# Kernel optimization log

Hardware: AMD Instinct MI355X
Metric: run time of the kernel (lower is better)

Reference implementation:

```python
import jax, jax.numpy as jnp
import numpy as np

B, LTEXT, LVIS, D, H = 16, 128, 4096, 1024, 16
HD = D // H


def setup_inputs() -> dict:
    key = jax.random.key(0)
    ks = jax.random.split(key, 8)
    s = 0.02
    return {
        'hidden_states': jax.random.normal(ks[0], (B, LVIS, D), jnp.float32),
        'text_states': jax.random.normal(ks[1], (LTEXT, B, D), jnp.float32),
        'Wq': jax.random.normal(ks[2], (D, D), jnp.float32) * s,
        'bq': jnp.zeros((D,), jnp.float32),
        'Wk': jax.random.normal(ks[3], (D, D), jnp.float32) * s,
        'bk': jnp.zeros((D,), jnp.float32),
        'Wv': jax.random.normal(ks[4], (D, D), jnp.float32) * s,
        'bv': jnp.zeros((D,), jnp.float32),
        'Wo': jax.random.normal(ks[5], (D, D), jnp.float32) * s,
        'bo': jnp.zeros((D,), jnp.float32),
    }


def reference(hidden_states, text_states, Wq, bq, Wk, bk, Wv, bv, Wo, bo):
    # text_states: (L_text, B, D) -- code unpacks text_len, bsz from dims 0,1
    # hidden_states: (B, L_vis, D) -- key/value source
    Ltext, bsz, d = text_states.shape
    Lvis = hidden_states.shape[1]
    scale = HD ** -0.5

    # projections (torch Linear x @ W.T + b, here W stored already transposed)
    q = (text_states @ Wq + bq) * scale
    # faithful to torch .view: flatten memory then reshape to (B, Ltext, H, hd)
    q = q.reshape(bsz, Ltext, H, HD).transpose(0, 2, 1, 3)        # (B,H,Lt,hd)
    k = (hidden_states @ Wk + bk).reshape(bsz, Lvis, H, HD).transpose(0, 2, 1, 3)
    v = (hidden_states @ Wv + bv).reshape(bsz, Lvis, H, HD).transpose(0, 2, 1, 3)

    attn = jax.nn.softmax(jnp.einsum('bhtd,bhsd->bhts', q, k), axis=-1)  # (B,H,Lt,Lv)
    text_guided_vision = jnp.einsum('bhts,bhsd->bhtd', attn, v)          # (B,H,Lt,hd)
    # second matmul with transposed attention weights: P^T @ (P V)
    out = jnp.einsum('bhts,bhtd->bhsd', attn, text_guided_vision)        # (B,H,Lv,hd)

    out = out.transpose(0, 2, 1, 3).reshape(bsz, Lvis, d)
    return out @ Wo + bo
```

## Files before the change

kernel.cpp:

```cpp
#include <hip/hip_runtime.h>
#include <stdint.h>

typedef short  s16x8 __attribute__((ext_vector_type(8)));
typedef float  f32x4 __attribute__((ext_vector_type(4)));
typedef unsigned short u16x4 __attribute__((ext_vector_type(4)));

__device__ __forceinline__ unsigned short f2bf(float f) {
  unsigned u = __builtin_bit_cast(unsigned, f);
  u = (u + 0x7fffu + ((u >> 16) & 1u)) >> 16;
  return (unsigned short)u;
}

__device__ __forceinline__ void glds16(const void* g, void* l) {
  __builtin_amdgcn_global_load_lds((const __attribute__((address_space(1))) void*)g,
                                   (__attribute__((address_space(3))) void*)l, 16, 0, 0);
}

__device__ __forceinline__ f32x4 mfma16(s16x8 a, s16x8 b, f32x4 c) {
  return __builtin_amdgcn_mfma_f32_16x16x32_bf16(a, b, c, 0, 0, 0);
}

#define VM4 asm volatile("s_waitcnt vmcnt(4)" ::: "memory")
#define VM0 asm volatile("s_waitcnt vmcnt(0)" ::: "memory")

__global__ __launch_bounds__(256) void kt_cvt(const float* __restrict__ X,
                                              unsigned short* __restrict__ Y) {
  const size_t N8 = (size_t)16 * 4096 * 1024 / 8;
  for (size_t i = (size_t)blockIdx.x * 256 + threadIdx.x; i < N8;
       i += (size_t)gridDim.x * 256) {
    const float* g = X + i * 8;
    f32x4 a = *(const f32x4*)g;
    f32x4 b = *(const f32x4*)(g + 4);
    s16x8 o;
    o[0]=f2bf(a[0]); o[1]=f2bf(a[1]); o[2]=f2bf(a[2]); o[3]=f2bf(a[3]);
    o[4]=f2bf(b[0]); o[5]=f2bf(b[1]); o[6]=f2bf(b[2]); o[7]=f2bf(b[3]);
    *(s16x8*)(Y + i * 8) = o;
  }
}

__global__ void kt_transpose(const float* __restrict__ W, unsigned short* __restrict__ WT) {
  __shared__ float tile[64][65];
  int n0 = blockIdx.x * 64, k0 = blockIdx.y * 64;
  int tx = threadIdx.x, ty = threadIdx.y;
  #pragma unroll
  for (int r = ty; r < 64; r += 4)
    tile[r][tx] = W[(size_t)(k0 + r) * 1024 + n0 + tx];
  __syncthreads();
  #pragma unroll
  for (int r = ty; r < 64; r += 4)
    WT[(size_t)(n0 + r) * 1024 + k0 + tx] = f2bf(tile[tx][r]);
}

__global__ __launch_bounds__(256, 2) void kt_gemm_q(
    const float* __restrict__ Ain, const unsigned short* __restrict__ BT,
    const float* __restrict__ bias, unsigned short* __restrict__ Cout) {
  __shared__ __align__(16) unsigned short As[128 * 32];
  __shared__ __align__(16) unsigned short Bs[128 * 32];
  const int tid = threadIdx.x, lane = tid & 63, wave = tid >> 6;
  const int l15 = lane & 15, quad = lane >> 4;
  const int wr = wave >> 1, wc = wave & 1;
  const int n0 = blockIdx.x * 128, m0 = blockIdx.y * 128;

  f32x4 acc[4][4] = {};
  for (int k0 = 0; k0 < 1024; k0 += 32) {
    __syncthreads();
    #pragma unroll
    for (int i = 0; i < 2; ++i) {
      int rowb = (wave * 2 + i) * 16 + (lane >> 2);
      glds16(BT + (size_t)(n0 + rowb) * 1024 + k0 + (lane & 3) * 8,
             &Bs[(wave * 2 + i) * 512]);
    }
    {
      const float* A = Ain;
      int row = tid >> 1, ks = (tid & 1) * 16;
      const float* g = &A[(size_t)(m0 + row) * 1024 + k0 + ks];
      f32x4 fa = *(const f32x4*)(g);
      f32x4 fb = *(const f32x4*)(g + 4);
      f32x4 fc = *(const f32x4*)(g + 8);
      f32x4 fd = *(const f32x4*)(g + 12);
      s16x8 lo, hi;
      lo[0]=f2bf(fa[0]); lo[1]=f2bf(fa[1]); lo[2]=f2bf(fa[2]); lo[3]=f2bf(fa[3]);
      lo[4]=f2bf(fb[0]); lo[5]=f2bf(fb[1]); lo[6]=f2bf(fb[2]); lo[7]=f2bf(fb[3]);
      hi[0]=f2bf(fc[0]); hi[1]=f2bf(fc[1]); hi[2]=f2bf(fc[2]); hi[3]=f2bf(fc[3]);
      hi[4]=f2bf(fd[0]); hi[5]=f2bf(fd[1]); hi[6]=f2bf(fd[2]); hi[7]=f2bf(fd[3]);
      *(s16x8*)&As[row * 32 + ks] = lo;
      *(s16x8*)&As[row * 32 + ks + 8] = hi;
    }
    __syncthreads();
    s16x8 a[4], b[4];
    #pragma unroll
    for (int i = 0; i < 4; ++i) a[i] = *(const s16x8*)&As[(wr * 64 + i * 16 + l15) * 32 + quad * 8];
    #pragma unroll
    for (int j = 0; j < 4; ++j) b[j] = *(const s16x8*)&Bs[(wc * 64 + j * 16 + l15) * 32 + quad * 8];
    #pragma unroll
    for (int i = 0; i < 4; ++i)
      #pragma unroll
      for (int j = 0; j < 4; ++j) acc[i][j] = mfma16(a[i], b[j], acc[i][j]);
  }
  #pragma unroll
  for (int j = 0; j < 4; ++j) {
    int col = n0 + wc * 64 + j * 16 + l15;
    float bv = bias[col];
    #pragma unroll
    for (int i = 0; i < 4; ++i)
      #pragma unroll
      for (int r = 0; r < 4; ++r) {
        int row = m0 + wr * 64 + i * 16 + quad * 4 + r;
        float v = (acc[i][j][r] + bv) * 0.125f;
        size_t idx = ((size_t)((row >> 7) * 16 + (col >> 6)) * 128 + (row & 127)) * 64 + (col & 63);
        Cout[idx] = f2bf(v);
      }
  }
}

template <int MODE>
__global__ __launch_bounds__(512, 2) void kt_gemm256(
    const unsigned short* __restrict__ A, const unsigned short* __restrict__ BT,
    const float* __restrict__ bias0, const float* __restrict__ bias1,
    void* __restrict__ out0, void* __restrict__ out1) {
  constexpr int NN = (MODE == 0) ? 8 : 4;
  constexpr int CHUNK = (MODE == 0) ? 256 : 128;
  __shared__ __align__(16) unsigned short lds[65536];
  const int tid = threadIdx.x, lane = tid & 63, wave = tid >> 6;
  const int l15 = lane & 15, quad = lane >> 4;
  const int wr = wave >> 2, wc = wave & 3;
  const int r0 = lane >> 3, sck = (lane & 7) ^ r0;
  const int bid = blockIdx.x;
  const int logical = (bid & 7) * CHUNK + (bid >> 3);
  const int nblk = logical & (NN - 1), mblk = logical / NN;
  const int n0 = nblk * 256, m0 = mblk * 256;
  const unsigned short* Asrc = A + (size_t)m0 * 1024;
  const unsigned short* Bsrc = BT + (size_t)n0 * 1024;

  f32x4 acc[8][4] = {};
  s16x8 bf_[4][2];

  auto stageA = [&](int t, int h, int buf) {
    #pragma unroll
    for (int is = 0; is < 2; ++is) {
      int c = wave * 2 + is;
      glds16(Asrc + (size_t)(h * 128 + c * 8 + r0) * 1024 + t * 64 + sck * 8,
             &lds[buf * 32768 + h * 8192 + c * 512]);
    }
  };
  auto stageB = [&](int t, int h, int buf) {
    #pragma unroll
    for (int is = 0; is < 2; ++is) {
      int c = wave * 2 + is;
      glds16(Bsrc + (size_t)(h * 128 + c * 8 + r0) * 1024 + t * 64 + sck * 8,
             &lds[buf * 32768 + 16384 + h * 8192 + c * 512]);
    }
  };

  stageA(0, 0, 0); stageA(0, 1, 0); stageB(0, 0, 0); stageB(0, 1, 0);
  stageB(1, 0, 1); stageB(1, 1, 1);
  VM4;
  __builtin_amdgcn_s_barrier();

  #pragma unroll 1
  for (int it = 0; it < 8; ++it) {
    const bool last = (it == 7);
    const int te = 2 * it;
    #pragma unroll
    for (int half = 0; half < 2; ++half) {
      const int buf = half;
      #pragma unroll
      for (int p = 0; p < 4; ++p) {
        if (p == 0) {
          #pragma unroll
          for (int j = 0; j < 4; ++j)
            #pragma unroll
            for (int kk = 0; kk < 2; ++kk) {
              int r = (wc & 1) * 64 + j * 16 + l15;
              bf_[j][kk] = *(const s16x8*)&lds[buf * 32768 + 16384 + (wc >> 1) * 8192
                                               + r * 64 + (((kk * 4 + quad) ^ (r & 7)) << 3)];
            }
        }
        s16x8 af[2][2];
        #pragma unroll
        for (int ii = 0; ii < 2; ++ii)
          #pragma unroll
          for (int kk = 0; kk < 2; ++kk) {
            int r = (p * 2 + ii) * 16 + l15;
            af[ii][kk] = *(const s16x8*)&lds[buf * 32768 + wr * 8192
                                             + r * 64 + (((kk * 4 + quad) ^ (r & 7)) << 3)];
          }
        if (half == 0) {
          if (p == 0) { stageA(te + 1, 0, 1); stageA(te + 1, 1, 1); }
          else if (p == 1) { if (!last) stageB(te + 2, 0, 0); }
          else if (p == 2) { if (!last) stageB(te + 2, 1, 0); }
        } else {
          if (p == 0) { if (!last) stageA(te + 2, 0, 0); }
          else if (p == 1) { if (!last) { stageA(te + 2, 1, 0); stageB(te + 3, 0, 1); } }
          else if (p == 2) { if (!last) stageB(te + 3, 1, 1); }
        }
        __builtin_amdgcn_s_barrier();
        __builtin_amdgcn_s_setprio(1);
        #pragma unroll
        for (int ii = 0; ii < 2; ++ii)
          #pragma unroll
          for (int j = 0; j < 4; ++j)
            #pragma unroll
            for (int kk = 0; kk < 2; ++kk)
              acc[p * 2 + ii][j] = mfma16(af[ii][kk], bf_[j][kk], acc[p * 2 + ii][j]);
        __builtin_amdgcn_s_setprio(0);
        if (p == 3) {
          if (half == 0) { if (last) { VM0; } else { VM4; } }
          else           { if (!last) { VM4; } }
        }
        __builtin_amdgcn_s_barrier();
      }
    }
  }

  const int bb = m0 >> 12;
  const bool isV = (MODE == 0) && (n0 >= 1024);
  const float* bias = isV ? bias1 : bias0;
  #pragma unroll
  for (int j = 0; j < 4; ++j) {
    const int colg = n0 + wc * 64 + j * 16 + l15;
    const int c1 = colg & 1023;
    const float bv = bias[c1];
    const int hcol = c1 >> 6, dcol = c1 & 63;
    #pragma unroll
    for (int i = 0; i < 8; ++i) {
      const int row0 = m0 + wr * 128 + i * 16 + quad * 4;
      const int s = row0 & 4095;
      if constexpr (MODE == 0) {
        if (isV) {
          size_t base = (((size_t)bb * 16 + hcol) * 64 + dcol) * 4096 + s;
          u16x4 w;
          #pragma unroll
          for (int r = 0; r < 4; ++r) w[r] = f2bf(acc[i][j][r] + bv);
          *(u16x4*)&((unsigned short*)out1)[base] = w;
        } else {
          unsigned short* Ko = (unsigned short*)out0;
          size_t base = (((size_t)bb * 16 + hcol) * 4096 + s) * 64 + dcol;
          #pragma unroll
          for (int r = 0; r < 4; ++r) Ko[base + (size_t)r * 64] = f2bf(acc[i][j][r] + bv);
        }
      } else {
        float* O = (float*)out0;
        size_t base = (size_t)row0 * 1024 + colg;
        #pragma unroll
        for (int r = 0; r < 4; ++r) O[base + (size_t)r * 1024] = acc[i][j][r] + bv;
      }
    }
  }
}

__global__ __launch_bounds__(256, 2) void kt_attn1(
    const unsigned short* __restrict__ Qb, const unsigned short* __restrict__ Kb,
    const unsigned short* __restrict__ Vt, float* __restrict__ RpT,
    float* __restrict__ Zp) {
  __shared__ __align__(16) unsigned short Ks[128 * 64];
  __shared__ __align__(16) unsigned short Vts[64 * 128];
  __shared__ __align__(16) unsigned short Es[128 * 128];
  const int tid = threadIdx.x, lane = tid & 63, wave = tid >> 6;
  const int l15 = lane & 15, quad = lane >> 4;
  const int bid = blockIdx.x;
  const int lid = (bid & 7) * 128 + (bid >> 3);
  const int qidx = lid & 3, bh = lid >> 2;
  const size_t kbase = (size_t)bh * 4096 * 64;
  const size_t vbase = (size_t)bh * 64 * 4096;
  s16x8 qa[2][2];
  #pragma unroll
  for (int i = 0; i < 2; ++i)
    #pragma unroll
    for (int kk = 0; kk < 2; ++kk)
      qa[i][kk] = *(const s16x8*)&Qb[((size_t)bh * 128 + wave * 32 + i * 16 + l15) * 64 + kk * 32 + quad * 8];
  s16x8 bones;
  { unsigned short o = (l15 == 0) ? (unsigned short)0x3F80 : (unsigned short)0;
    #pragma unroll
    for (int c2 = 0; c2 < 8; ++c2) bones[c2] = (short)o; }
  f32x4 Racc[2][4] = {};
  f32x4 Zacc[2] = {};
  for (int ch = 0; ch < 8; ++ch) {
    const int s0 = qidx * 1024 + ch * 128;
    __syncthreads();
    #pragma unroll
    for (int i = 0; i < 4; ++i) {
      int srow = (wave * 4 + i) * 8 + (lane >> 3);
      glds16(Kb + kbase + (size_t)(s0 + srow) * 64 + (lane & 7) * 8, &Ks[(wave * 4 + i) * 512]);
    }
    #pragma unroll
    for (int i = 0; i < 4; ++i) {
      int drow = (wave * 4 + i) * 4 + (lane >> 4);
      glds16(Vt + vbase + (size_t)drow * 4096 + s0 + (lane & 15) * 8, &Vts[(wave * 4 + i) * 512]);
    }
    __syncthreads();
    f32x4 Sacc[2][8] = {};
    #pragma unroll
    for (int kk = 0; kk < 2; ++kk) {
      s16x8 bk_[8];
      #pragma unroll
      for (int j = 0; j < 8; ++j)
        bk_[j] = *(const s16x8*)&Ks[(j * 16 + l15) * 64 + kk * 32 + quad * 8];
      #pragma unroll
      for (int i = 0; i < 2; ++i)
        #pragma unroll
        for (int j = 0; j < 8; ++j) Sacc[i][j] = mfma16(qa[i][kk], bk_[j], Sacc[i][j]);
    }
    #pragma unroll
    for (int i = 0; i < 2; ++i)
      #pragma unroll
      for (int j = 0; j < 8; ++j)
        #pragma unroll
        for (int r = 0; r < 4; ++r)
          Es[(wave * 32 + i * 16 + quad * 4 + r) * 128 + j * 16 + l15] = f2bf(__expf(Sacc[i][j][r]));
    #pragma unroll
    for (int kk = 0; kk < 4; ++kk) {
      s16x8 ea[2];
      #pragma unroll
      for (int i2 = 0; i2 < 2; ++i2)
        ea[i2] = *(const s16x8*)&Es[(wave * 32 + i2 * 16 + l15) * 128 + kk * 32 + quad * 8];
      s16x8 bv_[4];
      #pragma unroll
      for (int jd = 0; jd < 4; ++jd)
        bv_[jd] = *(const s16x8*)&Vts[(jd * 16 + l15) * 128 + kk * 32 + quad * 8];
      #pragma unroll
      for (int i2 = 0; i2 < 2; ++i2) {
        #pragma unroll
        for (int jd = 0; jd < 4; ++jd) Racc[i2][jd] = mfma16(ea[i2], bv_[jd], Racc[i2][jd]);
        Zacc[i2] = mfma16(ea[i2], bones, Zacc[i2]);
      }
    }
  }
  #pragma unroll
  for (int i2 = 0; i2 < 2; ++i2) {
    int t0 = wave * 32 + i2 * 16 + quad * 4;
    #pragma unroll
    for (int jd = 0; jd < 4; ++jd) {
      int d = jd * 16 + l15;
      *(f32x4*)&RpT[(((size_t)qidx * 256 + bh) * 64 + d) * 128 + t0] = Racc[i2][jd];
    }
    if (l15 == 0) {
      #pragma unroll
      for (int r = 0; r < 4; ++r)
        Zp[((size_t)qidx * 256 + bh) * 128 + t0 + r] = Zacc[i2][r];
    }
  }
}

__global__ void kt_reduce(const float* __restrict__ RpT, const float* __restrict__ Zp,
                          unsigned short* __restrict__ Gt) {
  size_t id = (size_t)blockIdx.x * 256 + threadIdx.x;
  int t = (int)(id & 127);
  size_t bh = id >> 13;
  float z = 0.f, r = 0.f;
  #pragma unroll
  for (int q = 0; q < 4; ++q) {
    z += Zp[(size_t)q * 32768 + bh * 128 + t];
    r += RpT[(size_t)q * 2097152 + id];
  }
  Gt[id] = f2bf(r / (z * z));
}

__global__ __launch_bounds__(256, 2) void kt_attn2(
    const unsigned short* __restrict__ Qb, const unsigned short* __restrict__ Kb,
    const unsigned short* __restrict__ Gt, unsigned short* __restrict__ Ao) {
  __shared__ __align__(16) unsigned short Ks[64 * 64];
  __shared__ __align__(16) unsigned short EsT[64 * 136];
  const int tid = threadIdx.x, lane = tid & 63, wave = tid >> 6;
  const int l15 = lane & 15, quad = lane >> 4;
  const int bid = blockIdx.x;
  const int lid = (bid & 7) * 128 + (bid >> 3);
  const int c = lid & 3, bh = lid >> 2;
  const int h = bh & 15, b = bh >> 4;
  s16x8 qf[8][2], gf[4][4];
  #pragma unroll
  for (int jt = 0; jt < 8; ++jt)
    #pragma unroll
    for (int kk = 0; kk < 2; ++kk)
      qf[jt][kk] = *(const s16x8*)&Qb[((size_t)bh * 128 + jt * 16 + l15) * 64 + kk * 32 + quad * 8];
  #pragma unroll
  for (int jd = 0; jd < 4; ++jd)
    #pragma unroll
    for (int kk = 0; kk < 4; ++kk)
      gf[jd][kk] = *(const s16x8*)&Gt[((size_t)bh * 64 + jd * 16 + l15) * 128 + kk * 32 + quad * 8];
  const size_t kbase = (size_t)bh * 4096 * 64;
  for (int it = 0; it < 16; ++it) {
    const int s0 = c * 1024 + it * 64;
    __syncthreads();
    #pragma unroll
    for (int i = 0; i < 2; ++i) {
      int srow = (wave * 2 + i) * 8 + (lane >> 3);
      glds16(Kb + kbase + (size_t)(s0 + srow) * 64 + (lane & 7) * 8, &Ks[(wave * 2 + i) * 512]);
    }
    __syncthreads();
    f32x4 Sacc[8] = {};
    #pragma unroll
    for (int kk = 0; kk < 2; ++kk) {
      s16x8 a = *(const s16x8*)&Ks[(wave * 16 + l15) * 64 + kk * 32 + quad * 8];
      #pragma unroll
      for (int jt = 0; jt < 8; ++jt) Sacc[jt] = mfma16(a, qf[jt][kk], Sacc[jt]);
    }
    #pragma unroll
    for (int jt = 0; jt < 8; ++jt)
      #pragma unroll
      for (int r = 0; r < 4; ++r)
        EsT[(wave * 16 + quad * 4 + r) * 136 + jt * 16 + l15] = f2bf(__expf(Sacc[jt][r]));
    f32x4 Oacc[4] = {};
    #pragma unroll
    for (int kk = 0; kk < 4; ++kk) {
      s16x8 ea = *(const s16x8*)&EsT[(wave * 16 + l15) * 136 + kk * 32 + quad * 8];
      #pragma unroll
      for (int jd = 0; jd < 4; ++jd) Oacc[jd] = mfma16(ea, gf[jd][kk], Oacc[jd]);
    }
    #pragma unroll
    for (int jd = 0; jd < 4; ++jd)
      #pragma unroll
      for (int r = 0; r < 4; ++r) {
        int s = s0 + wave * 16 + quad * 4 + r;
        int d = jd * 16 + l15;
        Ao[((size_t)b * 4096 + s) * 1024 + h * 64 + d] = f2bf(Oacc[jd][r]);
      }
  }
}

extern "C" void kernel_launch(void* const* d_in, const int* in_sizes, int n_in,
                              void* d_out, int out_size, void* d_ws, size_t ws_size,
                              hipStream_t stream) {
  const float* hidden = (const float*)d_in[0];
  const float* text   = (const float*)d_in[1];
  const float* Wq = (const float*)d_in[2]; const float* bq = (const float*)d_in[3];
  const float* Wk = (const float*)d_in[4]; const float* bk = (const float*)d_in[5];
  const float* Wv = (const float*)d_in[6]; const float* bv = (const float*)d_in[7];
  const float* Wo = (const float*)d_in[8]; const float* bo = (const float*)d_in[9];
  char* ws = (char*)d_ws;
  unsigned short* WqT = (unsigned short*)(ws + (size_t)0);
  unsigned short* WkT = (unsigned short*)(ws + ((size_t)2 << 20));
  unsigned short* WvT = (unsigned short*)(ws + ((size_t)4 << 20));
  unsigned short* WoT = (unsigned short*)(ws + ((size_t)6 << 20));
  unsigned short* Qb  = (unsigned short*)(ws + ((size_t)8 << 20));
  unsigned short* Kb  = (unsigned short*)(ws + ((size_t)12 << 20));
  unsigned short* Vt  = (unsigned short*)(ws + ((size_t)140 << 20));
  unsigned short* Hb  = (unsigned short*)(ws + ((size_t)268 << 20));
  unsigned short* Ao  = (unsigned short*)(ws + ((size_t)268 << 20));
  float*          RpT = (float*)(ws + ((size_t)396 << 20));
  float*          Zp  = (float*)(ws + ((size_t)428 << 20));
  unsigned short* Gt  = (unsigned short*)(ws + ((size_t)429 << 20));

  dim3 blk(256);
  kt_transpose<<<dim3(16, 16), dim3(64, 4), 0, stream>>>(Wq, WqT);
  kt_transpose<<<dim3(16, 16), dim3(64, 4), 0, stream>>>(Wk, WkT);
  kt_transpose<<<dim3(16, 16), dim3(64, 4), 0, stream>>>(Wv, WvT);
  kt_transpose<<<dim3(16, 16), dim3(64, 4), 0, stream>>>(Wo, WoT);
  kt_cvt<<<dim3(2048), blk, 0, stream>>>(hidden, Hb);
  kt_gemm_q<<<dim3(8, 16), blk, 0, stream>>>(text, WqT, bq, Qb);
  kt_gemm256<0><<<dim3(2048), dim3(512), 0, stream>>>(Hb, WkT, bk, bv, Kb, Vt);
  kt_attn1<<<dim3(1024), blk, 0, stream>>>(Qb, Kb, Vt, RpT, Zp);
  kt_reduce<<<dim3(8192), blk, 0, stream>>>(RpT, Zp, Gt);
  kt_attn2<<<dim3(1024), blk, 0, stream>>>(Qb, Kb, Gt, Ao);
  kt_gemm256<2><<<dim3(1024), dim3(512), 0, stream>>>(Ao, WoT, bo, nullptr, d_out, nullptr);
}
```

Measured before the change: 1.196 ms.

## Double-buffer K/V staging with XOR swizzle in attention kernels, widen attn1 to 8 waves

Both attention kernels now stage the next K (and V) chunk into a second LDS buffer while computing on the current one, replacing the two barriers per iteration with one wait and one barrier. LDS tiles use an XOR swizzle on 16-byte chunks to reduce bank conflicts on fragment reads. attn1 moves from 4 to 8 waves per block, each wave owning 16 query rows, and uses a small per-wave exp buffer instead of a full 128x128 tile. This cuts registers and LDS per wave so more waves can be resident, at the cost of more LDS for the double buffers.

```diff
diff --git a/kernel.cpp b/kernel.cpp
--- a/kernel.cpp
+++ b/kernel.cpp
@@ -249,13 +249,13 @@
   }
 }
 
-__global__ __launch_bounds__(256, 2) void kt_attn1(
+__global__ __launch_bounds__(512, 4) void kt_attn1(
     const unsigned short* __restrict__ Qb, const unsigned short* __restrict__ Kb,
     const unsigned short* __restrict__ Vt, float* __restrict__ RpT,
     float* __restrict__ Zp) {
-  __shared__ __align__(16) unsigned short Ks[128 * 64];
-  __shared__ __align__(16) unsigned short Vts[64 * 128];
-  __shared__ __align__(16) unsigned short Es[128 * 128];
+  __shared__ __align__(16) unsigned short Ks[2][128 * 64];
+  __shared__ __align__(16) unsigned short Vts[2][64 * 128];
+  __shared__ __align__(16) unsigned short Es[8][16 * 40];
   const int tid = threadIdx.x, lane = tid & 63, wave = tid >> 6;
   const int l15 = lane & 15, quad = lane >> 4;
   const int bid = blockIdx.x;
@@ -263,82 +263,91 @@
   const int qidx = lid & 3, bh = lid >> 2;
   const size_t kbase = (size_t)bh * 4096 * 64;
   const size_t vbase = (size_t)bh * 64 * 4096;
-  s16x8 qa[2][2];
-  #pragma unroll
-  for (int i = 0; i < 2; ++i)
-    #pragma unroll
-    for (int kk = 0; kk < 2; ++kk)
-      qa[i][kk] = *(const s16x8*)&Qb[((size_t)bh * 128 + wave * 32 + i * 16 + l15) * 64 + kk * 32 + quad * 8];
+  s16x8 qa[2];
+  #pragma unroll
+  for (int kk = 0; kk < 2; ++kk)
+    qa[kk] = *(const s16x8*)&Qb[((size_t)bh * 128 + wave * 16 + l15) * 64 + kk * 32 + quad * 8];
   s16x8 bones;
   { unsigned short o = (l15 == 0) ? (unsigned short)0x3F80 : (unsigned short)0;
     #pragma unroll
     for (int c2 = 0; c2 < 8; ++c2) bones[c2] = (short)o; }
-  f32x4 Racc[2][4] = {};
-  f32x4 Zacc[2] = {};
+  f32x4 Racc[4] = {};
+  f32x4 Zacc = {};
+
+  auto stage = [&](int ch, int buf) {
+    const int s0 = qidx * 1024 + ch * 128;
+    #pragma unroll
+    for (int i = 0; i < 2; ++i) {
+      int srow = wave * 16 + i * 8 + (lane >> 3);
+      int ck = (lane & 7) ^ (srow & 7);
+      glds16(Kb + kbase + (size_t)(s0 + srow) * 64 + ck * 8,
+             &Ks[buf][(wave * 16 + i * 8) * 64]);
+    }
+    #pragma unroll
+    for (int i = 0; i < 2; ++i) {
+      int drow = wave * 8 + i * 4 + (lane >> 4);
+      int ck = (lane & 15) ^ (drow & 15);
+      glds16(Vt + vbase + (size_t)drow * 4096 + s0 + ck * 8,
+             &Vts[buf][(wave * 8 + i * 4) * 128]);
+    }
+  };
+
+  stage(0, 0);
+  VM0;
+  __syncthreads();
+
+  #pragma unroll 1
   for (int ch = 0; ch < 8; ++ch) {
-    const int s0 = qidx * 1024 + ch * 128;
+    const int buf = ch & 1;
+    if (ch < 7) stage(ch + 1, buf ^ 1);
+    f32x4 Sacc[8] = {};
+    #pragma unroll
+    for (int kk = 0; kk < 2; ++kk)
+      #pragma unroll
+      for (int jh = 0; jh < 2; ++jh) {
+        s16x8 bk[4];
+        #pragma unroll
+        for (int j = 0; j < 4; ++j) {
+          int r = (jh * 4 + j) * 16 + l15;
+          bk[j] = *(const s16x8*)&Ks[buf][r * 64 + (((kk * 4 + quad) ^ (r & 7)) << 3)];
+        }
+        #pragma unroll
+        for (int j = 0; j < 4; ++j)
+          Sacc[jh * 4 + j] = mfma16(qa[kk], bk[j], Sacc[jh * 4 + j]);
+      }
+    #pragma unroll
+    for (int kk2 = 0; kk2 < 4; ++kk2) {
+      #pragma unroll
+      for (int jl = 0; jl < 2; ++jl) {
+        int j = kk2 * 2 + jl;
+        #pragma unroll
+        for (int r = 0; r < 4; ++r)
+          Es[wave][(quad * 4 + r) * 40 + jl * 16 + l15] = f2bf(__expf(Sacc[j][r]));
+      }
+      s16x8 ea = *(const s16x8*)&Es[wave][l15 * 40 + quad * 8];
+      s16x8 bv[4];
+      #pragma unroll
+      for (int jd = 0; jd < 4; ++jd) {
+        int r = jd * 16 + l15;
+        bv[jd] = *(const s16x8*)&Vts[buf][r * 128 + (((kk2 * 4 + quad) ^ (r & 15)) << 3)];
+      }
+      #pragma unroll
+      for (int jd = 0; jd < 4; ++jd) Racc[jd] = mfma16(ea, bv[jd], Racc[jd]);
+      Zacc = mfma16(ea, bones, Zacc);
+    }
+    if (ch < 7) VM0;
     __syncthreads();
-    #pragma unroll
-    for (int i = 0; i < 4; ++i) {
-      int srow = (wave * 4 + i) * 8 + (lane >> 3);
-      glds16(Kb + kbase + (size_t)(s0 + srow) * 64 + (lane & 7) * 8, &Ks[(wave * 4 + i) * 512]);
-    }
-    #pragma unroll
-    for (int i = 0; i < 4; ++i) {
-      int drow = (wave * 4 + i) * 4 + (lane >> 4);
-      glds16(Vt + vbase + (size_t)drow * 4096 + s0 + (lane & 15) * 8, &Vts[(wave * 4 + i) * 512]);
-    }
-    __syncthreads();
-    f32x4 Sacc[2][8] = {};
-    #pragma unroll
-    for (int kk = 0; kk < 2; ++kk) {
-      s16x8 bk_[8];
-      #pragma unroll
-      for (int j = 0; j < 8; ++j)
-        bk_[j] = *(const s16x8*)&Ks[(j * 16 + l15) * 64 + kk * 32 + quad * 8];
-      #pragma unroll
-      for (int i = 0; i < 2; ++i)
-        #pragma unroll
-        for (int j = 0; j < 8; ++j) Sacc[i][j] = mfma16(qa[i][kk], bk_[j], Sacc[i][j]);
-    }
-    #pragma unroll
-    for (int i = 0; i < 2; ++i)
-      #pragma unroll
-      for (int j = 0; j < 8; ++j)
-        #pragma unroll
-        for (int r = 0; r < 4; ++r)
-          Es[(wave * 32 + i * 16 + quad * 4 + r) * 128 + j * 16 + l15] = f2bf(__expf(Sacc[i][j][r]));
-    #pragma unroll
-    for (int kk = 0; kk < 4; ++kk) {
-      s16x8 ea[2];
-      #pragma unroll
-      for (int i2 = 0; i2 < 2; ++i2)
-        ea[i2] = *(const s16x8*)&Es[(wave * 32 + i2 * 16 + l15) * 128 + kk * 32 + quad * 8];
-      s16x8 bv_[4];
-      #pragma unroll
-      for (int jd = 0; jd < 4; ++jd)
-        bv_[jd] = *(const s16x8*)&Vts[(jd * 16 + l15) * 128 + kk * 32 + quad * 8];
-      #pragma unroll
-      for (int i2 = 0; i2 < 2; ++i2) {
-        #pragma unroll
-        for (int jd = 0; jd < 4; ++jd) Racc[i2][jd] = mfma16(ea[i2], bv_[jd], Racc[i2][jd]);
-        Zacc[i2] = mfma16(ea[i2], bones, Zacc[i2]);
-      }
-    }
-  }
-  #pragma unroll
-  for (int i2 = 0; i2 < 2; ++i2) {
-    int t0 = wave * 32 + i2 * 16 + quad * 4;
-    #pragma unroll
-    for (int jd = 0; jd < 4; ++jd) {
-      int d = jd * 16 + l15;
-      *(f32x4*)&RpT[(((size_t)qidx * 256 + bh) * 64 + d) * 128 + t0] = Racc[i2][jd];
-    }
-    if (l15 == 0) {
-      #pragma unroll
-      for (int r = 0; r < 4; ++r)
-        Zp[((size_t)qidx * 256 + bh) * 128 + t0 + r] = Zacc[i2][r];
-    }
+  }
+  int t0 = wave * 16 + quad * 4;
+  #pragma unroll
+  for (int jd = 0; jd < 4; ++jd) {
+    int d = jd * 16 + l15;
+    *(f32x4*)&RpT[(((size_t)qidx * 256 + bh) * 64 + d) * 128 + t0] = Racc[jd];
+  }
+  if (l15 == 0) {
+    #pragma unroll
+    for (int r = 0; r < 4; ++r)
+      Zp[((size_t)qidx * 256 + bh) * 128 + t0 + r] = Zacc[r];
   }
 }
 
@@ -359,7 +368,7 @@
 __global__ __launch_bounds__(256, 2) void kt_attn2(
     const unsigned short* __restrict__ Qb, const unsigned short* __restrict__ Kb,
     const unsigned short* __restrict__ Gt, unsigned short* __restrict__ Ao) {
-  __shared__ __align__(16) unsigned short Ks[64 * 64];
+  __shared__ __align__(16) unsigned short Ks[2][64 * 64];
   __shared__ __align__(16) unsigned short EsT[64 * 136];
   const int tid = threadIdx.x, lane = tid & 63, wave = tid >> 6;
   const int l15 = lane & 15, quad = lane >> 4;
@@ -379,19 +388,32 @@
     for (int kk = 0; kk < 4; ++kk)
       gf[jd][kk] = *(const s16x8*)&Gt[((size_t)bh * 64 + jd * 16 + l15) * 128 + kk * 32 + quad * 8];
   const size_t kbase = (size_t)bh * 4096 * 64;
+
+  auto stage = [&](int it, int buf) {
+    const int s0 = c * 1024 + it * 64;
+    #pragma unroll
+    for (int i = 0; i < 2; ++i) {
+      int srow = wave * 16 + i * 8 + (lane >> 3);
+      int ck = (lane & 7) ^ (srow & 7);
+      glds16(Kb + kbase + (size_t)(s0 + srow) * 64 + ck * 8,
+             &Ks[buf][(wave * 16 + i * 8) * 64]);
+    }
+  };
+
+  stage(0, 0);
+  VM0;
+  __syncthreads();
+
+  #pragma unroll 1
   for (int it = 0; it < 16; ++it) {
+    const int buf = it & 1;
+    if (it < 15) stage(it + 1, buf ^ 1);
     const int s0 = c * 1024 + it * 64;
-    __syncthreads();
-    #pragma unroll
-    for (int i = 0; i < 2; ++i) {
-      int srow = (wave * 2 + i) * 8 + (lane >> 3);
-      glds16(Kb + kbase + (size_t)(s0 + srow) * 64 + (lane & 7) * 8, &Ks[(wave * 2 + i) * 512]);
-    }
-    __syncthreads();
     f32x4 Sacc[8] = {};
     #pragma unroll
     for (int kk = 0; kk < 2; ++kk) {
-      s16x8 a = *(const s16x8*)&Ks[(wave * 16 + l15) * 64 + kk * 32 + quad * 8];
+      int r = wave * 16 + l15;
+      s16x8 a = *(const s16x8*)&Ks[buf][r * 64 + (((kk * 4 + quad) ^ (r & 7)) << 3)];
       #pragma unroll
       for (int jt = 0; jt < 8; ++jt) Sacc[jt] = mfma16(a, qf[jt][kk], Sacc[jt]);
     }
@@ -415,6 +437,8 @@
         int d = jd * 16 + l15;
         Ao[((size_t)b * 4096 + s) * 1024 + h * 64 + d] = f2bf(Oacc[jd][r]);
       }
+    if (it < 15) VM0;
+    __syncthreads();
   }
 }
 
@@ -449,7 +473,7 @@
   kt_cvt<<<dim3(2048), blk, 0, stream>>>(hidden, Hb);
   kt_gemm_q<<<dim3(8, 16), blk, 0, stream>>>(text, WqT, bq, Qb);
   kt_gemm256<0><<<dim3(2048), dim3(512), 0, stream>>>(Hb, WkT, bk, bv, Kb, Vt);
-  kt_attn1<<<dim3(1024), blk, 0, stream>>>(Qb, Kb, Vt, RpT, Zp);
+  kt_attn1<<<dim3(1024), dim3(512), 0, stream>>>(Qb, Kb, Vt, RpT, Zp);
   kt_reduce<<<dim3(8192), blk, 0, stream>>>(RpT, Zp, Gt);
   kt_attn2<<<dim3(1024), blk, 0, stream>>>(Qb, Kb, Gt, Ao);
   kt_gemm256<2><<<dim3(1024), dim3(512), 0, stream>>>(Ao, WoT, bo, nullptr, d_out, nullptr);
```

New measurement: 1.161 ms. 2.9% less time.
